# Performance work log

Hardware: AMD Instinct MI355X
Metric: run time of the kernel (lower is better)

## Reference

```python
import jax, jax.numpy as jnp
import numpy as np

NQ = 4        # nqubits
NLAYERS = 2   # nlayers
DIM = 2 ** NQ # statevector size = 16


def _apply_1q(state, U, wire, batched):
    """Apply a single-qubit gate U on `wire` to state [B, 16].
    U is [B,2,2] if batched else [2,2]. Pennylane wire 0 = most significant bit."""
    B = state.shape[0]
    st = state.reshape((B,) + (2,) * NQ)
    ax = wire + 1
    st = jnp.moveaxis(st, ax, -1).reshape(B, DIM // 2, 2)
    if batched:
        st = jnp.einsum('bij,bkj->bki', U, st)
    else:
        st = jnp.einsum('ij,bkj->bki', U, st)
    st = st.reshape((B,) + (2,) * NQ)  # last axis is the wire axis now
    st = jnp.moveaxis(st, -1, ax)
    return st.reshape(B, DIM)


def _apply_cnot(state, c, t):
    """CNOT with control c, target t on state [B, 16]."""
    B = state.shape[0]
    st = state.reshape((B,) + (2,) * NQ)
    cax, tax = c + 1, t + 1
    s0 = jnp.take(st, 0, axis=cax)  # control=0 slice, axis removed
    s1 = jnp.take(st, 1, axis=cax)  # control=1 slice
    s1 = jnp.flip(s1, axis=tax - (1 if tax > cax else 0))  # X on target
    st = jnp.stack([s0, s1], axis=cax)
    return st.reshape(B, DIM)


def _simulate(angles, qnn_weights):
    """Batched 4-qubit circuit: RX(angles) encoding, then NLAYERS of
    [RY(weights) on each wire, CNOT ring]. Returns <Z_i> per wire: [B, 4]."""
    B = angles.shape[0]
    state = jnp.zeros((B, DIM), dtype=jnp.complex64).at[:, 0].set(1.0)

    # RX encoding (per-sample angles)
    c = jnp.cos(angles / 2)
    s = jnp.sin(angles / 2)
    for w in range(NQ):
        row0 = jnp.stack([c[:, w] + 0j, -1j * s[:, w]], axis=-1)
        row1 = jnp.stack([-1j * s[:, w], c[:, w] + 0j], axis=-1)
        U = jnp.stack([row0, row1], axis=-2)  # [B,2,2] complex64
        state = _apply_1q(state, U, w, batched=True)

    # Entangling layers (shared weights)
    cw = jnp.cos(qnn_weights / 2)
    sw = jnp.sin(qnn_weights / 2)
    for layer in range(NLAYERS):
        for w in range(NQ):
            k = w + layer * NQ
            U = jnp.stack([jnp.stack([cw[k], -sw[k]]),
                           jnp.stack([sw[k], cw[k]])]).astype(jnp.complex64)
            state = _apply_1q(state, U, w, batched=False)
        for w in range(NQ):
            state = _apply_cnot(state, w, (w + 1) % NQ)

    # <Z_i> = P(bit_i = 0) - P(bit_i = 1)
    probs = jnp.abs(state) ** 2  # [B, 16] real float32
    pr = probs.reshape((B,) + (2,) * NQ)
    evs = []
    for w in range(NQ):
        axes = tuple(a for a in range(1, NQ + 1) if a != w + 1)
        marg = pr.sum(axis=axes)  # [B, 2]
        evs.append(marg[:, 0] - marg[:, 1])
    return jnp.stack(evs, axis=-1)  # [B, 4]


def setup_inputs() -> dict:
    key = jax.random.key(0)
    ks = jax.random.split(key, 6)
    B = 131072
    x = jax.random.uniform(ks[0], (B, 28, 28), dtype=jnp.float32) * 255.0
    W_red = jax.random.normal(ks[1], (NQ, 28 * 28), dtype=jnp.float32) * 0.03
    b_red = jax.random.normal(ks[2], (NQ,), dtype=jnp.float32) * 0.01
    qnn_weights = jax.random.uniform(ks[3], (NLAYERS * NQ,), dtype=jnp.float32) * np.pi
    W_out = jax.random.normal(ks[4], (10, NQ), dtype=jnp.float32) * 0.3
    b_out = jax.random.normal(ks[5], (10,), dtype=jnp.float32) * 0.01
    return {"x": x, "W_red": W_red, "b_red": b_red,
            "qnn_weights": qnn_weights, "W_out": W_out, "b_out": b_out}


def reference(x, W_red, b_red, qnn_weights, W_out, b_out):
    B = x.shape[0]
    h = x.reshape(B, -1) / 255.0
    h = h @ W_red.T + b_red                 # [B, 4]
    angles = jnp.tanh(h) * jnp.pi           # [B, 4]
    ev = _simulate(angles, qnn_weights)     # [B, 4]
    return ev @ W_out.T + b_out             # [B, 10]
```

## Files before the change

kernel.cpp:

```cpp
#include <hip/hip_runtime.h>
#include <math.h>

#define PI_F 3.14159265358979323846f

__device__ __forceinline__ float dot4(const float4 a, const float4 b) {
    return a.x * b.x + a.y * b.y + a.z * b.z + a.w * b.w;
}

template<int P>
__device__ __forceinline__ void rx_gate(float (&ar)[16], float (&ai)[16], float c, float s) {
#pragma unroll
    for (int m = 0; m < 8; ++m) {
        const int i0 = ((m >> P) << (P + 1)) | (m & ((1 << P) - 1));
        const int i1 = i0 | (1 << P);
        const float a0r = ar[i0], a0i = ai[i0], a1r = ar[i1], a1i = ai[i1];
        ar[i0] = c * a0r + s * a1i;
        ai[i0] = c * a0i - s * a1r;
        ar[i1] = c * a1r + s * a0i;
        ai[i1] = c * a1i - s * a0r;
    }
}

template<int P>
__device__ __forceinline__ void ry_gate(float (&ar)[16], float (&ai)[16], float c, float s) {
#pragma unroll
    for (int m = 0; m < 8; ++m) {
        const int i0 = ((m >> P) << (P + 1)) | (m & ((1 << P) - 1));
        const int i1 = i0 | (1 << P);
        const float a0r = ar[i0], a0i = ai[i0], a1r = ar[i1], a1i = ai[i1];
        ar[i0] = c * a0r - s * a1r;
        ai[i0] = c * a0i - s * a1i;
        ar[i1] = s * a0r + c * a1r;
        ai[i1] = s * a0i + c * a1i;
    }
}

template<int PC, int PT>
__device__ __forceinline__ void cnot_gate(float (&ar)[16], float (&ai)[16]) {
#pragma unroll
    for (int i = 0; i < 16; ++i) {
        if ((i & (1 << PC)) && !(i & (1 << PT))) {
            const int j = i | (1 << PT);
            float tr = ar[i]; ar[i] = ar[j]; ar[j] = tr;
            float ti = ai[i]; ai[i] = ai[j]; ai[j] = ti;
        }
    }
}

__global__ __launch_bounds__(256, 4)
void hybrid_qnn_kernel(const float* __restrict__ x,
                       const float* __restrict__ W_red,
                       const float* __restrict__ b_red,
                       const float* __restrict__ qw,
                       const float* __restrict__ W_out,
                       const float* __restrict__ b_out,
                       float* __restrict__ out,
                       int B)
{
    __shared__ float h_lds[64][4];
    __shared__ float qc_lds[8];
    __shared__ float qs_lds[8];
    __shared__ float outStage[640];

    const int t = threadIdx.x;
    const int lane = t & 63;
    const int wave = t >> 6;
    const long long blockBase = (long long)blockIdx.x * 64;

    if (t < 8) {
        const float a = 0.5f * qw[t];
        qc_lds[t] = cosf(a);
        qs_lds[t] = sinf(a);
    }

    const float inv255 = 1.0f / 255.0f;
    float4 Wl[3][4];
#pragma unroll
    for (int c = 0; c < 3; ++c) {
#pragma unroll
        for (int j = 0; j < 4; ++j) {
            const float4 w = *(const float4*)(W_red + j * 784 + 4 * (lane + 64 * c));
            Wl[c][j] = make_float4(w.x * inv255, w.y * inv255, w.z * inv255, w.w * inv255);
        }
    }
    float4 Wr[4];
#pragma unroll
    for (int j = 0; j < 4; ++j) Wr[j] = make_float4(0.f, 0.f, 0.f, 0.f);
    if (lane < 4) {
#pragma unroll
        for (int j = 0; j < 4; ++j) {
            const float4 w = *(const float4*)(W_red + j * 784 + 4 * (192 + lane));
            Wr[j] = make_float4(w.x * inv255, w.y * inv255, w.z * inv255, w.w * inv255);
        }
    }
    const float br0 = b_red[0], br1 = b_red[1], br2 = b_red[2], br3 = b_red[3];

#pragma unroll 2
    for (int q = 0; q < 16; ++q) {
        const int srow = wave * 16 + q;
        const long long samp = blockBase + srow;
        if (samp < B) {
            const float4* xr4 = (const float4*)(x + (size_t)samp * 784);
            const float4 x0 = xr4[lane];
            const float4 x1 = xr4[lane + 64];
            const float4 x2 = xr4[lane + 128];
            float4 x3 = make_float4(0.f, 0.f, 0.f, 0.f);
            if (lane < 4) x3 = xr4[192 + lane];

            float s0 = dot4(x0, Wl[0][0]) + dot4(x1, Wl[1][0]) + dot4(x2, Wl[2][0]) + dot4(x3, Wr[0]);
            float s1 = dot4(x0, Wl[0][1]) + dot4(x1, Wl[1][1]) + dot4(x2, Wl[2][1]) + dot4(x3, Wr[1]);
            float s2 = dot4(x0, Wl[0][2]) + dot4(x1, Wl[1][2]) + dot4(x2, Wl[2][2]) + dot4(x3, Wr[2]);
            float s3 = dot4(x0, Wl[0][3]) + dot4(x1, Wl[1][3]) + dot4(x2, Wl[2][3]) + dot4(x3, Wr[3]);

#pragma unroll
            for (int m = 32; m >= 1; m >>= 1) {
                s0 += __shfl_xor(s0, m);
                s1 += __shfl_xor(s1, m);
                s2 += __shfl_xor(s2, m);
                s3 += __shfl_xor(s3, m);
            }
            if (lane == 0) {
                h_lds[srow][0] = s0 + br0;
                h_lds[srow][1] = s1 + br1;
                h_lds[srow][2] = s2 + br2;
                h_lds[srow][3] = s3 + br3;
            }
        }
    }
    __syncthreads();

    if (t < 64 && blockBase + t < B) {
        const float ang0 = tanhf(h_lds[t][0]) * PI_F;
        const float ang1 = tanhf(h_lds[t][1]) * PI_F;
        const float ang2 = tanhf(h_lds[t][2]) * PI_F;
        const float ang3 = tanhf(h_lds[t][3]) * PI_F;
        const float c0 = cosf(0.5f * ang0), sn0 = sinf(0.5f * ang0);
        const float c1 = cosf(0.5f * ang1), sn1 = sinf(0.5f * ang1);
        const float c2 = cosf(0.5f * ang2), sn2 = sinf(0.5f * ang2);
        const float c3 = cosf(0.5f * ang3), sn3 = sinf(0.5f * ang3);

        float ar[16], ai[16];
#pragma unroll
        for (int i = 0; i < 16; ++i) { ar[i] = 0.f; ai[i] = 0.f; }
        ar[0] = 1.f;

        rx_gate<3>(ar, ai, c0, sn0);
        rx_gate<2>(ar, ai, c1, sn1);
        rx_gate<1>(ar, ai, c2, sn2);
        rx_gate<0>(ar, ai, c3, sn3);

#pragma unroll
        for (int layer = 0; layer < 2; ++layer) {
            const int k0 = layer * 4;
            ry_gate<3>(ar, ai, qc_lds[k0 + 0], qs_lds[k0 + 0]);
            ry_gate<2>(ar, ai, qc_lds[k0 + 1], qs_lds[k0 + 1]);
            ry_gate<1>(ar, ai, qc_lds[k0 + 2], qs_lds[k0 + 2]);
            ry_gate<0>(ar, ai, qc_lds[k0 + 3], qs_lds[k0 + 3]);
            cnot_gate<3, 2>(ar, ai);
            cnot_gate<2, 1>(ar, ai);
            cnot_gate<1, 0>(ar, ai);
            cnot_gate<0, 3>(ar, ai);
        }

        float pr[16];
#pragma unroll
        for (int i = 0; i < 16; ++i) pr[i] = ar[i] * ar[i] + ai[i] * ai[i];

        float ev[4];
#pragma unroll
        for (int w = 0; w < 4; ++w) {
            const int p = 3 - w;
            float e = 0.f;
#pragma unroll
            for (int i = 0; i < 16; ++i) e += (i & (1 << p)) ? -pr[i] : pr[i];
            ev[w] = e;
        }

#pragma unroll
        for (int n = 0; n < 10; ++n) {
            float o = b_out[n];
#pragma unroll
            for (int j = 0; j < 4; ++j) o += ev[j] * W_out[n * 4 + j];
            outStage[t * 10 + n] = o;
        }
    }
    __syncthreads();

    const long long outBase = (long long)blockIdx.x * 640;
    const long long outTotal = (long long)B * 10;
#pragma unroll
    for (int i = t; i < 640; i += 256) {
        const long long oi = outBase + i;
        if (oi < outTotal) out[oi] = outStage[i];
    }
}

extern "C" void kernel_launch(void* const* d_in, const int* in_sizes, int n_in,
                              void* d_out, int out_size, void* d_ws, size_t ws_size,
                              hipStream_t stream) {
    const float* x      = (const float*)d_in[0];
    const float* W_red  = (const float*)d_in[1];
    const float* b_red  = (const float*)d_in[2];
    const float* qw     = (const float*)d_in[3];
    const float* W_out  = (const float*)d_in[4];
    const float* b_out  = (const float*)d_in[5];
    float* out = (float*)d_out;

    const int B = in_sizes[0] / 784;
    const int grid = (B + 63) / 64;
    hipLaunchKernelGGL(hybrid_qnn_kernel, dim3(grid), dim3(256), 0, stream,
                       x, W_red, b_red, qw, W_out, b_out, out, B);
}
```

Before: 86.91 us.

## Software-pipeline row loads, pack 4-way shuffle reduction, split tail columns

The per-row reduction loop now prefetches the next sample's three float4 loads before computing the current one, so memory latency overlaps with the FMAs. The four separate 6-step butterfly reductions are replaced by a packed reduction in which lanes exchange partial sums, cutting shuffle count roughly fourfold. The 16-element tail (columns 768-783) is handled once for all 16 samples of a wave, with four lanes per sample, instead of lanes 0-3 per row. This adds register pressure from the prefetch buffers and an LDS read-modify-write per row.

Result: faster. 81.20 us (-6.6%).

```diff
diff --git a/kernel.cpp b/kernel.cpp
--- a/kernel.cpp
+++ b/kernel.cpp
@@ -45,6 +45,19 @@
             float ti = ai[i]; ai[i] = ai[j]; ai[j] = ti;
         }
     }
+}
+
+__device__ __forceinline__ float pack_reduce4(int lane, float s0, float s1, float s2, float s3) {
+    const bool b1 = (lane & 1) != 0;
+    const bool b2 = (lane & 2) != 0;
+    const float u01 = (b1 ? s1 : s0) + __shfl_xor(b1 ? s0 : s1, 1);
+    const float u23 = (b1 ? s3 : s2) + __shfl_xor(b1 ? s2 : s3, 1);
+    float v = (b2 ? u23 : u01) + __shfl_xor(b2 ? u01 : u23, 2);
+    v += __shfl_xor(v, 4);
+    v += __shfl_xor(v, 8);
+    v += __shfl_xor(v, 16);
+    v += __shfl_xor(v, 32);
+    return v;
 }
 
 __global__ __launch_bounds__(256, 4)
@@ -66,6 +79,7 @@
     const int lane = t & 63;
     const int wave = t >> 6;
     const long long blockBase = (long long)blockIdx.x * 64;
+    const long long wbase = blockBase + wave * 16;
 
     if (t < 8) {
         const float a = 0.5f * qw[t];
@@ -74,6 +88,7 @@
     }
 
     const float inv255 = 1.0f / 255.0f;
+
     float4 Wl[3][4];
 #pragma unroll
     for (int c = 0; c < 3; ++c) {
@@ -83,48 +98,72 @@
             Wl[c][j] = make_float4(w.x * inv255, w.y * inv255, w.z * inv255, w.w * inv255);
         }
     }
-    float4 Wr[4];
-#pragma unroll
-    for (int j = 0; j < 4; ++j) Wr[j] = make_float4(0.f, 0.f, 0.f, 0.f);
-    if (lane < 4) {
+    const float br0 = b_red[0], br1 = b_red[1], br2 = b_red[2], br3 = b_red[3];
+
+    {
+        const int s = lane >> 2;
+        const int c = lane & 3;
+        const long long samp = wbase + s;
+        float4 wt[4];
 #pragma unroll
         for (int j = 0; j < 4; ++j) {
-            const float4 w = *(const float4*)(W_red + j * 784 + 4 * (192 + lane));
-            Wr[j] = make_float4(w.x * inv255, w.y * inv255, w.z * inv255, w.w * inv255);
-        }
-    }
-    const float br0 = b_red[0], br1 = b_red[1], br2 = b_red[2], br3 = b_red[3];
-
-#pragma unroll 2
-    for (int q = 0; q < 16; ++q) {
-        const int srow = wave * 16 + q;
-        const long long samp = blockBase + srow;
-        if (samp < B) {
-            const float4* xr4 = (const float4*)(x + (size_t)samp * 784);
-            const float4 x0 = xr4[lane];
-            const float4 x1 = xr4[lane + 64];
-            const float4 x2 = xr4[lane + 128];
-            float4 x3 = make_float4(0.f, 0.f, 0.f, 0.f);
-            if (lane < 4) x3 = xr4[192 + lane];
-
-            float s0 = dot4(x0, Wl[0][0]) + dot4(x1, Wl[1][0]) + dot4(x2, Wl[2][0]) + dot4(x3, Wr[0]);
-            float s1 = dot4(x0, Wl[0][1]) + dot4(x1, Wl[1][1]) + dot4(x2, Wl[2][1]) + dot4(x3, Wr[1]);
-            float s2 = dot4(x0, Wl[0][2]) + dot4(x1, Wl[1][2]) + dot4(x2, Wl[2][2]) + dot4(x3, Wr[2]);
-            float s3 = dot4(x0, Wl[0][3]) + dot4(x1, Wl[1][3]) + dot4(x2, Wl[2][3]) + dot4(x3, Wr[3]);
-
-#pragma unroll
-            for (int m = 32; m >= 1; m >>= 1) {
-                s0 += __shfl_xor(s0, m);
-                s1 += __shfl_xor(s1, m);
-                s2 += __shfl_xor(s2, m);
-                s3 += __shfl_xor(s3, m);
+            const float4 w = *(const float4*)(W_red + j * 784 + 768 + 4 * c);
+            wt[j] = make_float4(w.x * inv255, w.y * inv255, w.z * inv255, w.w * inv255);
+        }
+        float4 xt = make_float4(0.f, 0.f, 0.f, 0.f);
+        if (samp < B) xt = *(const float4*)(x + (size_t)samp * 784 + 768 + 4 * c);
+        float d0 = dot4(xt, wt[0]);
+        float d1 = dot4(xt, wt[1]);
+        float d2 = dot4(xt, wt[2]);
+        float d3 = dot4(xt, wt[3]);
+        d0 += __shfl_xor(d0, 1); d0 += __shfl_xor(d0, 2);
+        d1 += __shfl_xor(d1, 1); d1 += __shfl_xor(d1, 2);
+        d2 += __shfl_xor(d2, 1); d2 += __shfl_xor(d2, 2);
+        d3 += __shfl_xor(d3, 1); d3 += __shfl_xor(d3, 2);
+        if (c == 0 && samp < B) {
+            const int srow = wave * 16 + s;
+            h_lds[srow][0] = d0 + br0;
+            h_lds[srow][1] = d1 + br1;
+            h_lds[srow][2] = d2 + br2;
+            h_lds[srow][3] = d3 + br3;
+        }
+    }
+
+    if (wbase + 16 <= B) {
+        const float* xbase = x + (size_t)wbase * 784;
+        float4 c0 = *(const float4*)(xbase + 4 * lane);
+        float4 c1 = *(const float4*)(xbase + 4 * (lane + 64));
+        float4 c2 = *(const float4*)(xbase + 4 * (lane + 128));
+#pragma unroll
+        for (int q = 0; q < 16; ++q) {
+            const float4 x0 = c0, x1 = c1, x2 = c2;
+            if (q < 15) {
+                const float* nb = xbase + (size_t)(q + 1) * 784;
+                c0 = *(const float4*)(nb + 4 * lane);
+                c1 = *(const float4*)(nb + 4 * (lane + 64));
+                c2 = *(const float4*)(nb + 4 * (lane + 128));
             }
-            if (lane == 0) {
-                h_lds[srow][0] = s0 + br0;
-                h_lds[srow][1] = s1 + br1;
-                h_lds[srow][2] = s2 + br2;
-                h_lds[srow][3] = s3 + br3;
-            }
+            const float s0 = dot4(x0, Wl[0][0]) + dot4(x1, Wl[1][0]) + dot4(x2, Wl[2][0]);
+            const float s1 = dot4(x0, Wl[0][1]) + dot4(x1, Wl[1][1]) + dot4(x2, Wl[2][1]);
+            const float s2 = dot4(x0, Wl[0][2]) + dot4(x1, Wl[1][2]) + dot4(x2, Wl[2][2]);
+            const float s3 = dot4(x0, Wl[0][3]) + dot4(x1, Wl[1][3]) + dot4(x2, Wl[2][3]);
+            const float v = pack_reduce4(lane, s0, s1, s2, s3);
+            if (lane < 4) h_lds[wave * 16 + q][lane] += v;
+        }
+    } else {
+        for (int q = 0; q < 16; ++q) {
+            const long long samp = wbase + q;
+            if (samp >= B) break;
+            const float* xb = x + (size_t)samp * 784;
+            const float4 x0 = *(const float4*)(xb + 4 * lane);
+            const float4 x1 = *(const float4*)(xb + 4 * (lane + 64));
+            const float4 x2 = *(const float4*)(xb + 4 * (lane + 128));
+            const float s0 = dot4(x0, Wl[0][0]) + dot4(x1, Wl[1][0]) + dot4(x2, Wl[2][0]);
+            const float s1 = dot4(x0, Wl[0][1]) + dot4(x1, Wl[1][1]) + dot4(x2, Wl[2][1]);
+            const float s2 = dot4(x0, Wl[0][2]) + dot4(x1, Wl[1][2]) + dot4(x2, Wl[2][2]);
+            const float s3 = dot4(x0, Wl[0][3]) + dot4(x1, Wl[1][3]) + dot4(x2, Wl[2][3]);
+            const float v = pack_reduce4(lane, s0, s1, s2, s3);
+            if (lane < 4) h_lds[wave * 16 + q][lane] += v;
         }
     }
     __syncthreads();
```
